# Kernel tuning notes

Hardware: AMD Instinct MI355X
Metric: run time of the kernel (lower is better)

The kernel has to match this reference:

```python
import jax, jax.numpy as jnp
import numpy as np

B, C, HW, NP, L, D, NH, OUT = 32, 3, 224, 14, 12, 768, 12, 1000
PS = HW // NP            # 16
IN_D = C * PS * PS       # 768
S = NP * NP + 1          # 197
DH = D // NH             # 64
MD = 4 * D               # 3072


def setup_inputs() -> dict:
    key = jax.random.key(0)
    ks = iter(jax.random.split(key, 32))
    g = lambda shape: jax.random.normal(next(ks), shape, dtype=jnp.float32) * 0.02
    return {
        "images": jax.random.normal(next(ks), (B, C, HW, HW), dtype=jnp.float32),
        "Wp": g((D, IN_D)), "bp": jnp.zeros((D,), jnp.float32),
        "cls": jax.random.normal(next(ks), (1, D), dtype=jnp.float32),
        "pos": jnp.zeros((S, D), jnp.float32),  # frozen zeros in original
        "ln1_g": jnp.ones((L, D), jnp.float32), "ln1_b": jnp.zeros((L, D), jnp.float32),
        "Wq": g((L, NH, DH, DH)), "bq": jnp.zeros((L, NH, DH), jnp.float32),
        "Wk": g((L, NH, DH, DH)), "bk": jnp.zeros((L, NH, DH), jnp.float32),
        "Wv": g((L, NH, DH, DH)), "bv": jnp.zeros((L, NH, DH), jnp.float32),
        "ln2_g": jnp.ones((L, D), jnp.float32), "ln2_b": jnp.zeros((L, D), jnp.float32),
        "W1": g((L, MD, D)), "b1": jnp.zeros((L, MD), jnp.float32),
        "W2": g((L, D, MD)), "b2": jnp.zeros((L, D), jnp.float32),
        "Wh": g((OUT, D)), "bh": jnp.zeros((OUT,), jnp.float32),
    }


def _layernorm(x, g, b, eps=1e-5):
    m = jnp.mean(x, axis=-1, keepdims=True)
    v = jnp.var(x, axis=-1, keepdims=True)
    return (x - m) * jax.lax.rsqrt(v + eps) * g + b


def reference(images, Wp, bp, cls, pos, ln1_g, ln1_b, Wq, bq, Wk, bk, Wv, bv,
              ln2_g, ln2_b, W1, b1, W2, b2, Wh, bh):
    n = images.shape[0]
    # patchify: flatten order is (c, ph, pw) per patch, matching torch .flatten()
    p = images.reshape(n, C, NP, PS, NP, PS).transpose(0, 2, 4, 1, 3, 5)
    p = p.reshape(n, NP * NP, IN_D)
    tokens = p @ Wp.T + bp                                    # [B, NP^2, D]
    tokens = jnp.concatenate([jnp.broadcast_to(cls, (n, 1, D)), tokens], axis=1)
    x = tokens + pos                                          # [B, S, D]

    scale = 1.0 / np.sqrt(DH)

    def block(x, prm):
        g1, b1n, wq, bqv, wk, bkv, wv, bvv, g2, b2n, w1, b1v, w2, b2v = prm
        h = _layernorm(x, g1, b1n)
        hh = h.reshape(n, S, NH, DH)                          # split heads
        q = jnp.einsum('bshd,hed->bshe', hh, wq) + bqv
        k = jnp.einsum('bshd,hed->bshe', hh, wk) + bkv
        v = jnp.einsum('bshd,hed->bshe', hh, wv) + bvv
        att = jax.nn.softmax(jnp.einsum('bqhe,bkhe->bhqk', q, k) * scale, axis=-1)
        o = jnp.einsum('bhqk,bkhe->bqhe', att, v).reshape(n, S, D)
        x = x + o
        h2 = _layernorm(x, g2, b2n)
        m = jax.nn.gelu(h2 @ w1.T + b1v, approximate=False) @ w2.T + b2v
        return x + m, None

    x, _ = jax.lax.scan(block, x,
                        (ln1_g, ln1_b, Wq, bq, Wk, bk, Wv, bv,
                         ln2_g, ln2_b, W1, b1, W2, b2))
    logits = x[:, 0] @ Wh.T + bh
    return jax.nn.softmax(logits, axis=-1)
```

## Files before the change

### kernel.cpp

```cpp
#include <hip/hip_runtime.h>
#include <math.h>
#include <stdint.h>

#define NBATCH 32
#define SEQ 197
#define DIM 768
#define NHEAD 12
#define DH 64
#define MDIM 3072
#define NLAYER 12
#define NPATCH 196
#define NOUT 1000
#define MROWS (NBATCH * SEQ)
#define SPLITK 2

typedef __bf16 bf16x8 __attribute__((ext_vector_type(8)));
typedef float f32x4 __attribute__((ext_vector_type(4)));

__device__ __forceinline__ unsigned short f2bf(float f) {
    unsigned u = __float_as_uint(f);
    unsigned r = u + 0x7fffu + ((u >> 16) & 1u);
    return (unsigned short)(r >> 16);
}

__device__ __forceinline__ f32x4 mfma16(bf16x8 a, bf16x8 b, f32x4 c) {
    return __builtin_amdgcn_mfma_f32_16x16x32_bf16(a, b, c, 0, 0, 0);
}

__device__ __forceinline__ void gload_lds16(const void* g, const void* lds) {
    __builtin_amdgcn_global_load_lds(
        (const __attribute__((address_space(1))) void*)(uintptr_t)g,
        (__attribute__((address_space(3))) void*)(uint32_t)(uintptr_t)lds,
        16, 0, 0);
}

#define WAIT_VMCNT_4() asm volatile("s_waitcnt vmcnt(4)" ::: "memory")
#define WAIT_VMCNT_0() asm volatile("s_waitcnt vmcnt(0)" ::: "memory")
#define BARRIER_RAW()                      \
    do {                                   \
        asm volatile("" ::: "memory");     \
        __builtin_amdgcn_s_barrier();      \
        asm volatile("" ::: "memory");     \
    } while (0)

__global__ __launch_bounds__(256) void cvt4(const float* __restrict__ src,
                                            unsigned short* __restrict__ dst, int n4) {
    int stride = gridDim.x * 256;
    for (int i = blockIdx.x * 256 + threadIdx.x; i < n4; i += stride) {
        float4 f = *(const float4*)(src + (size_t)i * 4);
        ushort4 o;
        o.x = f2bf(f.x); o.y = f2bf(f.y); o.z = f2bf(f.z); o.w = f2bf(f.w);
        *(ushort4*)(dst + (size_t)i * 4) = o;
    }
}

__global__ __launch_bounds__(256) void cvt_qkvw(const float* __restrict__ Wq,
                                                const float* __restrict__ Wk,
                                                const float* __restrict__ Wv,
                                                unsigned short* __restrict__ dst) {
    const int n = NLAYER * NHEAD * 3 * 64 * 64;
    int stride = gridDim.x * 256;
    for (int i = blockIdx.x * 256 + threadIdx.x; i < n; i += stride) {
        int d = i & 63, e = (i >> 6) & 63;
        int v = i >> 12;
        int t = v % 3, hh = (v / 3) % NHEAD, l = v / (3 * NHEAD);
        const float* src = (t == 0) ? Wq : (t == 1) ? Wk : Wv;
        dst[i] = f2bf(src[(((size_t)(l * NHEAD + hh)) * 64 + e) * 64 + d]);
    }
}

__global__ __launch_bounds__(256) void cls_pos_kernel(const float* __restrict__ cls,
                                                      const float* __restrict__ pos,
                                                      float* __restrict__ x) {
    int b = blockIdx.x, tid = threadIdx.x;
#pragma unroll
    for (int i = 0; i < 3; i++) {
        int c = tid + i * 256;
        x[(size_t)b * SEQ * DIM + c] = cls[c] + pos[c];
    }
}

__global__ __launch_bounds__(256) void gemm_patch_bf(const unsigned short* __restrict__ imgbf,
                                                     const unsigned short* __restrict__ wpbf,
                                                     const float* __restrict__ bp,
                                                     const float* __restrict__ pos,
                                                     float* __restrict__ x) {
    __shared__ __align__(16) unsigned short As[2][128 * 32];
    __shared__ __align__(16) unsigned short Bs[2][128 * 32];
    const int t = threadIdx.x, l = t & 63, w = t >> 6;
    const int bm = blockIdx.x * 128, bn = blockIdx.y * 128;
    const int wr = w >> 1, wc = w & 1;
    f32x4 acc[4][4] = {};

    const int ra0 = t >> 2, ka0 = (t & 3) * 8;
    const int ra1 = (t + 256) >> 2, ka1 = ((t + 256) & 3) * 8;
    int gm0 = bm + ra0, b0 = gm0 / NPATCH, p0 = gm0 % NPATCH;
    int gm1 = bm + ra1, b1 = gm1 / NPATCH, p1 = gm1 % NPATCH;
    const unsigned short* ib0 =
        imgbf + ((size_t)b0 * 3 * 224 + (size_t)(p0 / 14) * 16) * 224 + (p0 % 14) * 16;
    const unsigned short* ib1 =
        imgbf + ((size_t)b1 * 3 * 224 + (size_t)(p1 / 14) * 16) * 224 + (p1 % 14) * 16;
    const unsigned short* Br0 = wpbf + (size_t)(bn + ra0) * 768 + ka0;
    const unsigned short* Br1 = wpbf + (size_t)(bn + ra1) * 768 + ka1;
    const int lA0 = (0 * 256 + w * 64) * 8, lA1 = (1 * 256 + w * 64) * 8;
    const int lr = l & 15, lk = (l >> 4) * 8;

#define PATCH_STAGE(buf, k0)                                                   \
    {                                                                          \
        int kA0 = (k0) + ka0, kA1 = (k0) + ka1;                                \
        int c0 = kA0 >> 8, i0 = (kA0 >> 4) & 15, j0 = kA0 & 15;                \
        int c1 = kA1 >> 8, i1 = (kA1 >> 4) & 15, j1 = kA1 & 15;                \
        gload_lds16(ib0 + ((size_t)c0 * 224 + i0) * 224 + j0, As[buf] + lA0);  \
        gload_lds16(ib1 + ((size_t)c1 * 224 + i1) * 224 + j1, As[buf] + lA1);  \
        gload_lds16(Br0 + (k0), Bs[buf] + lA0);                                \
        gload_lds16(Br1 + (k0), Bs[buf] + lA1);                                \
    }

    PATCH_STAGE(0, 0);
    int cur = 0;
    for (int k0 = 0; k0 < 768; k0 += 32) {
        if (k0 + 32 < 768) {
            PATCH_STAGE(cur ^ 1, k0 + 32);
            WAIT_VMCNT_4();
        } else {
            WAIT_VMCNT_0();
        }
        BARRIER_RAW();
        bf16x8 a[4], bfr[4];
#pragma unroll
        for (int m = 0; m < 4; m++)
            a[m] = *(const bf16x8*)(As[cur] + (wr * 64 + m * 16 + lr) * 32 + lk);
#pragma unroll
        for (int n = 0; n < 4; n++)
            bfr[n] = *(const bf16x8*)(Bs[cur] + (wc * 64 + n * 16 + lr) * 32 + lk);
#pragma unroll
        for (int m = 0; m < 4; m++)
#pragma unroll
            for (int n = 0; n < 4; n++)
                acc[m][n] = mfma16(a[m], bfr[n], acc[m][n]);
        BARRIER_RAW();
        cur ^= 1;
    }
#undef PATCH_STAGE

#pragma unroll
    for (int m = 0; m < 4; m++) {
#pragma unroll
        for (int r = 0; r < 4; r++) {
            int gm = bm + wr * 64 + m * 16 + (l >> 4) * 4 + r;
            int b2 = gm / NPATCH, p2 = gm % NPATCH;
            size_t orow = (size_t)(b2 * SEQ + 1 + p2) * DIM;
#pragma unroll
            for (int n = 0; n < 4; n++) {
                int gn = bn + wc * 64 + n * 16 + lr;
                x[orow + gn] = acc[m][n][r] + bp[gn] + pos[(size_t)(1 + p2) * DIM + gn];
            }
        }
    }
}

template <int RES, int RED>
__global__ __launch_bounds__(256) void ln_wave(const float* __restrict__ x_in,
                                               const float* __restrict__ addv,
                                               float* __restrict__ x_out,
                                               unsigned short* __restrict__ h_out,
                                               const float* __restrict__ g,
                                               const float* __restrict__ bb,
                                               const float* __restrict__ parts,
                                               const float* __restrict__ badd) {
    int w = threadIdx.x >> 6, l = threadIdx.x & 63;
    size_t row = (size_t)blockIdx.x * 4 + w;
    const float* xr = x_in + row * DIM;
    float4 v[3];
    float s = 0.f;
#pragma unroll
    for (int u = 0; u < 3; u++) {
        int c = u * 256 + l * 4;
        v[u] = *(const float4*)(xr + c);
        if (RES) {
            float4 a4 = *(const float4*)(addv + row * DIM + c);
            v[u].x += a4.x; v[u].y += a4.y; v[u].z += a4.z; v[u].w += a4.w;
        }
        if (RED) {
            float4 b4 = *(const float4*)(badd + c);
            v[u].x += b4.x; v[u].y += b4.y; v[u].z += b4.z; v[u].w += b4.w;
#pragma unroll
            for (int kc = 0; kc < SPLITK; kc++) {
                float4 p4 = *(const float4*)(parts + ((size_t)kc * MROWS + row) * DIM + c);
                v[u].x += p4.x; v[u].y += p4.y; v[u].z += p4.z; v[u].w += p4.w;
            }
        }
        s += v[u].x + v[u].y + v[u].z + v[u].w;
    }
#pragma unroll
    for (int o = 1; o < 64; o <<= 1) s += __shfl_xor(s, o, 64);
    float mean = s * (1.0f / 768.0f);
    float s2 = 0.f;
#pragma unroll
    for (int u = 0; u < 3; u++) {
        float dx = v[u].x - mean, dy = v[u].y - mean, dz = v[u].z - mean, dw = v[u].w - mean;
        s2 += dx * dx + dy * dy + dz * dz + dw * dw;
    }
#pragma unroll
    for (int o = 1; o < 64; o <<= 1) s2 += __shfl_xor(s2, o, 64);
    float inv = rsqrtf(s2 * (1.0f / 768.0f) + 1e-5f);
#pragma unroll
    for (int u = 0; u < 3; u++) {
        int c = u * 256 + l * 4;
        float4 g4 = *(const float4*)(g + c);
        float4 b4 = *(const float4*)(bb + c);
        ushort4 o;
        o.x = f2bf((v[u].x - mean) * inv * g4.x + b4.x);
        o.y = f2bf((v[u].y - mean) * inv * g4.y + b4.y);
        o.z = f2bf((v[u].z - mean) * inv * g4.z + b4.z);
        o.w = f2bf((v[u].w - mean) * inv * g4.w + b4.w);
        *(ushort4*)(h_out + row * DIM + c) = o;
        if (RES || RED) *(float4*)(x_out + row * DIM + c) = v[u];
    }
}

__global__ __launch_bounds__(256) void reduceK(float* __restrict__ x,
                                               const float* __restrict__ parts,
                                               const float* __restrict__ badd) {
    int w = threadIdx.x >> 6, l = threadIdx.x & 63;
    size_t row = (size_t)blockIdx.x * 4 + w;
#pragma unroll
    for (int u = 0; u < 3; u++) {
        int c = u * 256 + l * 4;
        float4 v = *(const float4*)(x + row * DIM + c);
        float4 b4 = *(const float4*)(badd + c);
        v.x += b4.x; v.y += b4.y; v.z += b4.z; v.w += b4.w;
#pragma unroll
        for (int kc = 0; kc < SPLITK; kc++) {
            float4 p4 = *(const float4*)(parts + ((size_t)kc * MROWS + row) * DIM + c);
            v.x += p4.x; v.y += p4.y; v.z += p4.z; v.w += p4.w;
        }
        *(float4*)(x + row * DIM + c) = v;
    }
}

#define KS_OFF 0
#define QS_OFF 14400
#define VT_OFF 28800
#define RG_OFF 43648
#define WS_OFF (RG_OFF + 14400)

__global__ __launch_bounds__(512) void fused_attn(const unsigned short* __restrict__ hbf,
                                                  const unsigned short* __restrict__ wqkv,
                                                  const float* __restrict__ bq,
                                                  const float* __restrict__ bk,
                                                  const float* __restrict__ bv,
                                                  float* __restrict__ o) {
    __shared__ __align__(16) unsigned short lds[73344];
    const int b = blockIdx.x, hd = blockIdx.y;
    const int t = threadIdx.x, l = t & 63, w = t >> 6;
    const size_t base = ((size_t)b * SEQ) * DIM + hd * DH;
    const int lr = l & 15, lk4 = l >> 4;
    const unsigned short* wh = wqkv + (size_t)hd * 12288;

    for (int i = t; i < 197 * 16; i += 512) {
        int s = i >> 4, c4 = i & 15;
        ushort4 v4 = *(const ushort4*)(hbf + base + (size_t)s * DIM + c4 * 4);
        *(ushort4*)(lds + RG_OFF + s * 72 + c4 * 4) = v4;
    }
    if (t < 48) {
        int s = 197 + (t >> 4), c4 = t & 15;
        ushort4 z; z.x = 0; z.y = 0; z.z = 0; z.w = 0;
        *(ushort4*)(lds + RG_OFF + s * 72 + c4 * 4) = z;
    }
    for (int i = t; i < 192 * 16; i += 512) {
        int r = i >> 4, c4 = i & 15;
        ushort4 v4 = *(const ushort4*)(wh + (size_t)r * 64 + c4 * 4);
        *(ushort4*)(lds + WS_OFF + r * 72 + c4 * 4) = v4;
    }
    for (int i = t; i < 64 * 32; i += 512) {
        int d = i >> 5, s2 = 197 + (i & 31);
        if (s2 < 232) lds[VT_OFF + d * 232 + s2] = 0;
    }
    __syncthreads();

    for (int st = w; st < 13; st += 8) {
        bf16x8 a0 = *(const bf16x8*)(lds + RG_OFF + (st * 16 + lr) * 72 + lk4 * 8);
        bf16x8 a1 = *(const bf16x8*)(lds + RG_OFF + (st * 16 + lr) * 72 + 32 + lk4 * 8);
#pragma unroll
        for (int tt = 0; tt < 3; tt++) {
            const float* bias = (tt == 0) ? bq : (tt == 1) ? bk : bv;
#pragma unroll
            for (int et = 0; et < 4; et++) {
                int wrow = (tt * 64 + et * 16 + lr) * 72;
                bf16x8 b0 = *(const bf16x8*)(lds + WS_OFF + wrow + lk4 * 8);
                bf16x8 b1 = *(const bf16x8*)(lds + WS_OFF + wrow + 32 + lk4 * 8);
                f32x4 acc = {0.f, 0.f, 0.f, 0.f};
                acc = mfma16(a0, b0, acc);
                acc = mfma16(a1, b1, acc);
                int e = et * 16 + lr;
                float bval = bias[hd * 64 + e];
#pragma unroll
                for (int r = 0; r < 4; r++) {
                    int s = st * 16 + lk4 * 4 + r;
                    if (s < SEQ) {
                        unsigned short val = f2bf(acc[r] + bval);
                        if (tt == 0) lds[QS_OFF + s * 72 + e] = val;
                        else if (tt == 1) lds[KS_OFF + s * 72 + e] = val;
                        else lds[VT_OFF + e * 232 + s] = val;
                    }
                }
            }
        }
    }
    __syncthreads();

    const int Pb = RG_OFF + w * 3712;
    {
        int jj = 208 + lk4 * 4;
        lds[Pb + lr * 232 + jj + 0] = 0;
        lds[Pb + lr * 232 + jj + 1] = 0;
        lds[Pb + lr * 232 + jj + 2] = 0;
        lds[Pb + lr * 232 + jj + 3] = 0;
    }

    for (int qt = w; qt < 13; qt += 8) {
        int qrow = min(qt * 16 + lr, SEQ - 1);
        bf16x8 q0 = *(const bf16x8*)(lds + QS_OFF + qrow * 72 + lk4 * 8);
        bf16x8 q1 = *(const bf16x8*)(lds + QS_OFF + qrow * 72 + 32 + lk4 * 8);
        f32x4 st_[13];
#pragma unroll
        for (int jt = 0; jt < 13; jt++) st_[jt] = (f32x4){0.f, 0.f, 0.f, 0.f};
#pragma unroll
        for (int jt = 0; jt < 13; jt++) {
            int jrow = min(jt * 16 + lr, SEQ - 1);
            bf16x8 k0 = *(const bf16x8*)(lds + KS_OFF + jrow * 72 + lk4 * 8);
            bf16x8 k1 = *(const bf16x8*)(lds + KS_OFF + jrow * 72 + 32 + lk4 * 8);
            st_[jt] = mfma16(k0, q0, st_[jt]);
            st_[jt] = mfma16(k1, q1, st_[jt]);
        }
        float mx = -1e30f;
#pragma unroll
        for (int jt = 0; jt < 13; jt++)
#pragma unroll
            for (int r = 0; r < 4; r++) {
                int j = jt * 16 + lk4 * 4 + r;
                float sv = st_[jt][r] * 0.125f;
                st_[jt][r] = (j < SEQ) ? sv : -1e30f;
                mx = fmaxf(mx, st_[jt][r]);
            }
        mx = fmaxf(mx, __shfl_xor(mx, 16, 64));
        mx = fmaxf(mx, __shfl_xor(mx, 32, 64));
        float sum = 0.f;
#pragma unroll
        for (int jt = 0; jt < 13; jt++)
#pragma unroll
            for (int r = 0; r < 4; r++) {
                float p = __expf(st_[jt][r] - mx);
                st_[jt][r] = p;
                sum += p;
            }
        sum += __shfl_xor(sum, 16, 64);
        sum += __shfl_xor(sum, 32, 64);
        float inv = 1.0f / sum;
#pragma unroll
        for (int jt = 0; jt < 13; jt++) {
            ushort4 pk;
            pk.x = f2bf(st_[jt][0] * inv); pk.y = f2bf(st_[jt][1] * inv);
            pk.z = f2bf(st_[jt][2] * inv); pk.w = f2bf(st_[jt][3] * inv);
            *(ushort4*)(lds + Pb + lr * 232 + jt * 16 + lk4 * 4) = pk;
        }
        f32x4 acc[4] = {};
#pragma unroll
        for (int kt = 0; kt < 7; kt++) {
            bf16x8 pa = *(const bf16x8*)(lds + Pb + lr * 232 + kt * 32 + lk4 * 8);
#pragma unroll
            for (int nt = 0; nt < 4; nt++) {
                bf16x8 bv8 = *(const bf16x8*)(lds + VT_OFF + (nt * 16 + lr) * 232 + kt * 32 + lk4 * 8);
                acc[nt] = mfma16(pa, bv8, acc[nt]);
            }
        }
#pragma unroll
        for (int nt = 0; nt < 4; nt++)
#pragma unroll
            for (int r = 0; r < 4; r++) {
                int qq = qt * 16 + lk4 * 4 + r;
                if (qq < SEQ) o[base + (size_t)qq * DIM + nt * 16 + lr] = acc[nt][r];
            }
    }
}

template <int MODE, int SWAPXY>
__global__ __launch_bounds__(256) void gemm_bf(const unsigned short* __restrict__ A,
                                               const unsigned short* __restrict__ Bw,
                                               const float* __restrict__ bias,
                                               void* __restrict__ Cout,
                                               const float* __restrict__ res,
                                               int M, int N, int K) {
    __shared__ __align__(16) unsigned short As[2][128 * 32];
    __shared__ __align__(16) unsigned short Bs[2][128 * 32];
    const int t = threadIdx.x, l = t & 63, w = t >> 6;
    const int bm = (SWAPXY ? blockIdx.y : blockIdx.x) * 128;
    const int bn = (SWAPXY ? blockIdx.x : blockIdx.y) * 128;
    const int wr = w >> 1, wc = w & 1;
    f32x4 acc[4][4] = {};

    const int ra0 = t >> 2, ka0 = (t & 3) * 8;
    const int ra1 = (t + 256) >> 2, ka1 = ((t + 256) & 3) * 8;
    const unsigned short* Ar0 = A + (size_t)min(bm + ra0, M - 1) * K + ka0;
    const unsigned short* Ar1 = A + (size_t)min(bm + ra1, M - 1) * K + ka1;
    const unsigned short* Br0 = Bw + (size_t)(bn + ra0) * K + ka0;
    const unsigned short* Br1 = Bw + (size_t)(bn + ra1) * K + ka1;
    const int lo0 = (0 * 256 + w * 64) * 8, lo1 = (1 * 256 + w * 64) * 8;
    const int lr = l & 15, lk = (l >> 4) * 8;

    gload_lds16(Ar0, As[0] + lo0);
    gload_lds16(Ar1, As[0] + lo1);
    gload_lds16(Br0, Bs[0] + lo0);
    gload_lds16(Br1, Bs[0] + lo1);
    int cur = 0;
    for (int k0 = 0; k0 < K; k0 += 32) {
        if (k0 + 32 < K) {
            gload_lds16(Ar0 + k0 + 32, As[cur ^ 1] + lo0);
            gload_lds16(Ar1 + k0 + 32, As[cur ^ 1] + lo1);
            gload_lds16(Br0 + k0 + 32, Bs[cur ^ 1] + lo0);
            gload_lds16(Br1 + k0 + 32, Bs[cur ^ 1] + lo1);
            WAIT_VMCNT_4();
        } else {
            WAIT_VMCNT_0();
        }
        BARRIER_RAW();
        bf16x8 a[4], bfr[4];
#pragma unroll
        for (int m = 0; m < 4; m++)
            a[m] = *(const bf16x8*)(As[cur] + (wr * 64 + m * 16 + lr) * 32 + lk);
#pragma unroll
        for (int n = 0; n < 4; n++)
            bfr[n] = *(const bf16x8*)(Bs[cur] + (wc * 64 + n * 16 + lr) * 32 + lk);
#pragma unroll
        for (int m = 0; m < 4; m++)
#pragma unroll
            for (int n = 0; n < 4; n++)
                acc[m][n] = mfma16(a[m], bfr[n], acc[m][n]);
        BARRIER_RAW();
        cur ^= 1;
    }

#pragma unroll
    for (int m = 0; m < 4; m++) {
#pragma unroll
        for (int r = 0; r < 4; r++) {
            int gm = bm + wr * 64 + m * 16 + (l >> 4) * 4 + r;
            if (gm >= M) continue;
#pragma unroll
            for (int n = 0; n < 4; n++) {
                int gn = bn + wc * 64 + n * 16 + lr;
                float vb = acc[m][n][r] + bias[gn];
                if (MODE == 1) {
                    float gl = 0.5f * vb * (1.0f + erff(vb * 0.70710678118f));
                    ((unsigned short*)Cout)[(size_t)gm * N + gn] = f2bf(gl);
                } else {
                    ((float*)Cout)[(size_t)gm * N + gn] = vb + res[(size_t)gm * N + gn];
                }
            }
        }
    }
}

__global__ __launch_bounds__(256) void gemm_splitk(const unsigned short* __restrict__ A,
                                                   const unsigned short* __restrict__ Bw,
                                                   float* __restrict__ parts,
                                                   int M, int N, int KFULL) {
    __shared__ __align__(16) unsigned short As[2][128 * 32];
    __shared__ __align__(16) unsigned short Bs[2][128 * 32];
    const int t = threadIdx.x, l = t & 63, w = t >> 6;
    const int bm = blockIdx.x * 128, bn = blockIdx.y * 128;
    const int KC = KFULL / SPLITK;
    const int kbeg = blockIdx.z * KC;
    const int wr = w >> 1, wc = w & 1;
    f32x4 acc[4][4] = {};

    const int ra0 = t >> 2, ka0 = (t & 3) * 8;
    const int ra1 = (t + 256) >> 2, ka1 = ((t + 256) & 3) * 8;
    const unsigned short* Ar0 = A + (size_t)min(bm + ra0, M - 1) * KFULL + kbeg + ka0;
    const unsigned short* Ar1 = A + (size_t)min(bm + ra1, M - 1) * KFULL + kbeg + ka1;
    const unsigned short* Br0 = Bw + (size_t)(bn + ra0) * KFULL + kbeg + ka0;
    const unsigned short* Br1 = Bw + (size_t)(bn + ra1) * KFULL + kbeg + ka1;
    const int lo0 = (0 * 256 + w * 64) * 8, lo1 = (1 * 256 + w * 64) * 8;
    const int lr = l & 15, lk = (l >> 4) * 8;

    gload_lds16(Ar0, As[0] + lo0);
    gload_lds16(Ar1, As[0] + lo1);
    gload_lds16(Br0, Bs[0] + lo0);
    gload_lds16(Br1, Bs[0] + lo1);
    int cur = 0;
    for (int k0 = 0; k0 < KC; k0 += 32) {
        if (k0 + 32 < KC) {
            gload_lds16(Ar0 + k0 + 32, As[cur ^ 1] + lo0);
            gload_lds16(Ar1 + k0 + 32, As[cur ^ 1] + lo1);
            gload_lds16(Br0 + k0 + 32, Bs[cur ^ 1] + lo0);
            gload_lds16(Br1 + k0 + 32, Bs[cur ^ 1] + lo1);
            WAIT_VMCNT_4();
        } else {
            WAIT_VMCNT_0();
        }
        BARRIER_RAW();
        bf16x8 a[4], bfr[4];
#pragma unroll
        for (int m = 0; m < 4; m++)
            a[m] = *(const bf16x8*)(As[cur] + (wr * 64 + m * 16 + lr) * 32 + lk);
#pragma unroll
        for (int n = 0; n < 4; n++)
            bfr[n] = *(const bf16x8*)(Bs[cur] + (wc * 64 + n * 16 + lr) * 32 + lk);
#pragma unroll
        for (int m = 0; m < 4; m++)
#pragma unroll
            for (int n = 0; n < 4; n++)
                acc[m][n] = mfma16(a[m], bfr[n], acc[m][n]);
        BARRIER_RAW();
        cur ^= 1;
    }

    float* po = parts + (size_t)blockIdx.z * M * N;
#pragma unroll
    for (int m = 0; m < 4; m++) {
#pragma unroll
        for (int r = 0; r < 4; r++) {
            int gm = bm + wr * 64 + m * 16 + (l >> 4) * 4 + r;
            if (gm >= M) continue;
#pragma unroll
            for (int n = 0; n < 4; n++) {
                int gn = bn + wc * 64 + n * 16 + lr;
                po[(size_t)gm * N + gn] = acc[m][n][r];
            }
        }
    }
}

__global__ __launch_bounds__(256) void head_kernel(const float* __restrict__ x,
                                                   const float* __restrict__ Wh,
                                                   const float* __restrict__ bh,
                                                   float* __restrict__ logits) {
    __shared__ float xs[768];
    int b = blockIdx.x;
    int tid = threadIdx.x;
#pragma unroll
    for (int i = 0; i < 3; i++) xs[tid + i * 256] = x[(size_t)b * SEQ * DIM + tid + i * 256];
    __syncthreads();
    int wave = tid >> 6, lane = tid & 63;
    int o = blockIdx.y * 4 + wave;
    if (o < NOUT) {
        float acc = 0;
#pragma unroll
        for (int t = 0; t < 12; t++) {
            int d = lane + t * 64;
            acc = fmaf(xs[d], Wh[(size_t)o * DIM + d], acc);
        }
#pragma unroll
        for (int off = 32; off > 0; off >>= 1) acc += __shfl_down(acc, off, 64);
        if (lane == 0) logits[b * NOUT + o] = acc + bh[o];
    }
}

__global__ __launch_bounds__(256) void softmax_kernel(const float* __restrict__ logits,
                                                      float* __restrict__ out) {
    __shared__ float tmp[4];
    int b = blockIdx.x, tid = threadIdx.x;
    float vals[4];
    float mx = -1e30f;
#pragma unroll
    for (int i = 0; i < 4; i++) {
        int c = tid + i * 256;
        vals[i] = (c < NOUT) ? logits[b * NOUT + c] : -1e30f;
        mx = fmaxf(mx, vals[i]);
    }
#pragma unroll
    for (int o = 32; o > 0; o >>= 1) mx = fmaxf(mx, __shfl_down(mx, o, 64));
    int wave = tid >> 6, lane = tid & 63;
    __syncthreads();
    if (lane == 0) tmp[wave] = mx;
    __syncthreads();
    mx = fmaxf(fmaxf(tmp[0], tmp[1]), fmaxf(tmp[2], tmp[3]));
    float s = 0;
#pragma unroll
    for (int i = 0; i < 4; i++) {
        int c = tid + i * 256;
        if (c < NOUT) {
            vals[i] = __expf(vals[i] - mx);
            s += vals[i];
        } else vals[i] = 0.f;
    }
#pragma unroll
    for (int o = 32; o > 0; o >>= 1) s += __shfl_down(s, o, 64);
    __syncthreads();
    if (lane == 0) tmp[wave] = s;
    __syncthreads();
    s = tmp[0] + tmp[1] + tmp[2] + tmp[3];
    float invs = 1.0f / s;
#pragma unroll
    for (int i = 0; i < 4; i++) {
        int c = tid + i * 256;
        if (c < NOUT) out[b * NOUT + c] = vals[i] * invs;
    }
}

extern "C" void kernel_launch(void* const* d_in, const int* in_sizes, int n_in,
                              void* d_out, int out_size, void* d_ws, size_t ws_size,
                              hipStream_t stream) {
    const float* images = (const float*)d_in[0];
    const float* Wp   = (const float*)d_in[1];
    const float* bp   = (const float*)d_in[2];
    const float* cls  = (const float*)d_in[3];
    const float* pos  = (const float*)d_in[4];
    const float* ln1g = (const float*)d_in[5];
    const float* ln1b = (const float*)d_in[6];
    const float* Wq   = (const float*)d_in[7];
    const float* bq   = (const float*)d_in[8];
    const float* Wk   = (const float*)d_in[9];
    const float* bk   = (const float*)d_in[10];
    const float* Wv   = (const float*)d_in[11];
    const float* bv   = (const float*)d_in[12];
    const float* ln2g = (const float*)d_in[13];
    const float* ln2b = (const float*)d_in[14];
    const float* W1   = (const float*)d_in[15];
    const float* b1   = (const float*)d_in[16];
    const float* W2   = (const float*)d_in[17];
    const float* b2   = (const float*)d_in[18];
    const float* Wh   = (const float*)d_in[19];
    const float* bh   = (const float*)d_in[20];
    float* out = (float*)d_out;

    const size_t NX = (size_t)MROWS * DIM;
    const size_t NIMG = (size_t)NBATCH * 3 * 224 * 224;
    const size_t NW = (size_t)MDIM * DIM;

    char* p = (char*)d_ws;
    float* x      = (float*)p;            p += NX * 4;
    float* h      = (float*)p;            p += NX * 4;
    float* logits = (float*)p;            p += (size_t)NBATCH * NOUT * 4;
    unsigned short* hbf   = (unsigned short*)p; p += NX * 2;
    unsigned short* h2bf  = (unsigned short*)p; p += NX * 2;
    unsigned short* mid   = (unsigned short*)p; p += (size_t)MROWS * MDIM * 2;
    unsigned short* wqkvb = (unsigned short*)p; p += (size_t)NLAYER * NHEAD * 12288 * 2;
    unsigned short* imgbf = (unsigned short*)p; p += NIMG * 2;
    unsigned short* wpbf  = (unsigned short*)p; p += (size_t)DIM * DIM * 2;

    size_t used = (size_t)(p - (char*)d_ws);
    bool skq = ws_size >= used + (size_t)SPLITK * NX * 4;
    float* parts = (float*)p;
    if (skq) p += (size_t)SPLITK * NX * 4;
    used = (size_t)(p - (char*)d_ws);
    bool big = ws_size >= used + (size_t)2 * NLAYER * NW * 2;
    unsigned short* w1a = (unsigned short*)p;
    unsigned short* w2a = big ? w1a + (size_t)NLAYER * NW : w1a + NW;

    cls_pos_kernel<<<dim3(NBATCH), dim3(256), 0, stream>>>(cls, pos, x);
    cvt4<<<dim3(2048), dim3(256), 0, stream>>>(images, imgbf, (int)(NIMG / 4));
    cvt4<<<dim3(576), dim3(256), 0, stream>>>(Wp, wpbf, (int)(DIM * DIM / 4));
    cvt_qkvw<<<dim3(1024), dim3(256), 0, stream>>>(Wq, Wk, Wv, wqkvb);
    gemm_patch_bf<<<dim3(49, 6), dim3(256), 0, stream>>>(imgbf, wpbf, bp, pos, x);
    if (big) {
        cvt4<<<dim3(2048), dim3(256), 0, stream>>>(W1, w1a, (int)(NLAYER * NW / 4));
        cvt4<<<dim3(2048), dim3(256), 0, stream>>>(W2, w2a, (int)(NLAYER * NW / 4));
    }

    for (int l = 0; l < NLAYER; l++) {
        const unsigned short* wl1 = big ? w1a + (size_t)l * NW : w1a;
        const unsigned short* wl2 = big ? w2a + (size_t)l * NW : w2a;
        if (!big) {
            cvt4<<<dim3(2048), dim3(256), 0, stream>>>(W1 + (size_t)l * NW, w1a, (int)(NW / 4));
            cvt4<<<dim3(2048), dim3(256), 0, stream>>>(W2 + (size_t)l * NW, w1a + NW, (int)(NW / 4));
        }
        if (skq && l > 0) {
            ln_wave<0, 1><<<dim3(MROWS / 4), dim3(256), 0, stream>>>(
                x, nullptr, x, hbf, ln1g + l * DIM, ln1b + l * DIM, parts, b2 + (l - 1) * DIM);
        } else {
            ln_wave<0, 0><<<dim3(MROWS / 4), dim3(256), 0, stream>>>(
                x, nullptr, nullptr, hbf, ln1g + l * DIM, ln1b + l * DIM, nullptr, nullptr);
        }
        fused_attn<<<dim3(NBATCH, NHEAD), dim3(512), 0, stream>>>(
            hbf, wqkvb + (size_t)l * NHEAD * 12288,
            bq + l * NHEAD * DH, bk + l * NHEAD * DH, bv + l * NHEAD * DH, h);
        ln_wave<1, 0><<<dim3(MROWS / 4), dim3(256), 0, stream>>>(
            x, h, x, h2bf, ln2g + l * DIM, ln2b + l * DIM, nullptr, nullptr);
        gemm_bf<1, 1><<<dim3(24, 50), dim3(256), 0, stream>>>(
            h2bf, wl1, b1 + l * MDIM, mid, nullptr, MROWS, MDIM, DIM);
        if (skq) {
            gemm_splitk<<<dim3(50, 6, SPLITK), dim3(256), 0, stream>>>(
                mid, wl2, parts, MROWS, DIM, MDIM);
        } else {
            gemm_bf<2, 0><<<dim3(50, 6), dim3(256), 0, stream>>>(
                mid, wl2, b2 + l * DIM, x, x, MROWS, DIM, MDIM);
        }
    }
    if (skq) {
        reduceK<<<dim3(MROWS / 4), dim3(256), 0, stream>>>(x, parts, b2 + (NLAYER - 1) * DIM);
    }

    head_kernel<<<dim3(NBATCH, 250), dim3(256), 0, stream>>>(x, Wh, bh, logits);
    softmax_kernel<<<dim3(NBATCH), dim3(256), 0, stream>>>(logits, out);
}
```

Baseline: 2.257 ms.

## Compute only CLS token in final layer after attention

In the last layer only the CLS row feeds the classifier head. So the attention kernel computes queries and the output for the first query tile only. The second LayerNorm and both MLP GEMMs then run on just the 32 CLS rows, which are gathered with a row stride of SEQ. The final split-K reduction is folded into the head kernel, which removes the reduceK pass over all rows. This is legitimate dead-work elimination, but it depends on the split-K path being active and on the MLP GEMMs handling M=32 correctly.

```diff
diff --git a/kernel.cpp b/kernel.cpp
--- a/kernel.cpp
+++ b/kernel.cpp
@@ -167,10 +167,12 @@
                                                const float* __restrict__ g,
                                                const float* __restrict__ bb,
                                                const float* __restrict__ parts,
-                                               const float* __restrict__ badd) {
+                                               const float* __restrict__ badd,
+                                               int xmul) {
     int w = threadIdx.x >> 6, l = threadIdx.x & 63;
     size_t row = (size_t)blockIdx.x * 4 + w;
-    const float* xr = x_in + row * DIM;
+    size_t xrow = row * xmul;
+    const float* xr = x_in + xrow * DIM;
     float4 v[3];
     float s = 0.f;
 #pragma unroll
@@ -178,7 +180,7 @@
         int c = u * 256 + l * 4;
         v[u] = *(const float4*)(xr + c);
         if (RES) {
-            float4 a4 = *(const float4*)(addv + row * DIM + c);
+            float4 a4 = *(const float4*)(addv + xrow * DIM + c);
             v[u].x += a4.x; v[u].y += a4.y; v[u].z += a4.z; v[u].w += a4.w;
         }
         if (RED) {
@@ -215,27 +217,7 @@
         o.z = f2bf((v[u].z - mean) * inv * g4.z + b4.z);
         o.w = f2bf((v[u].w - mean) * inv * g4.w + b4.w);
         *(ushort4*)(h_out + row * DIM + c) = o;
-        if (RES || RED) *(float4*)(x_out + row * DIM + c) = v[u];
-    }
-}
-
-__global__ __launch_bounds__(256) void reduceK(float* __restrict__ x,
-                                               const float* __restrict__ parts,
-                                               const float* __restrict__ badd) {
-    int w = threadIdx.x >> 6, l = threadIdx.x & 63;
-    size_t row = (size_t)blockIdx.x * 4 + w;
-#pragma unroll
-    for (int u = 0; u < 3; u++) {
-        int c = u * 256 + l * 4;
-        float4 v = *(const float4*)(x + row * DIM + c);
-        float4 b4 = *(const float4*)(badd + c);
-        v.x += b4.x; v.y += b4.y; v.z += b4.z; v.w += b4.w;
-#pragma unroll
-        for (int kc = 0; kc < SPLITK; kc++) {
-            float4 p4 = *(const float4*)(parts + ((size_t)kc * MROWS + row) * DIM + c);
-            v.x += p4.x; v.y += p4.y; v.z += p4.z; v.w += p4.w;
-        }
-        *(float4*)(x + row * DIM + c) = v;
+        if (RES || RED) *(float4*)(x_out + xrow * DIM + c) = v[u];
     }
 }
 
@@ -245,6 +227,7 @@
 #define RG_OFF 43648
 #define WS_OFF (RG_OFF + 14400)
 
+template <int QTMAX>
 __global__ __launch_bounds__(512) void fused_attn(const unsigned short* __restrict__ hbf,
                                                   const unsigned short* __restrict__ wqkv,
                                                   const float* __restrict__ bq,
@@ -284,6 +267,7 @@
         bf16x8 a1 = *(const bf16x8*)(lds + RG_OFF + (st * 16 + lr) * 72 + 32 + lk4 * 8);
 #pragma unroll
         for (int tt = 0; tt < 3; tt++) {
+            if (QTMAX == 1 && tt == 0 && st >= QTMAX) continue;
             const float* bias = (tt == 0) ? bq : (tt == 1) ? bk : bv;
 #pragma unroll
             for (int et = 0; et < 4; et++) {
@@ -319,7 +303,7 @@
         lds[Pb + lr * 232 + jj + 3] = 0;
     }
 
-    for (int qt = w; qt < 13; qt += 8) {
+    for (int qt = w; qt < QTMAX; qt += 8) {
         int qrow = min(qt * 16 + lr, SEQ - 1);
         bf16x8 q0 = *(const bf16x8*)(lds + QS_OFF + qrow * 72 + lk4 * 8);
         bf16x8 q1 = *(const bf16x8*)(lds + QS_OFF + qrow * 72 + 32 + lk4 * 8);
@@ -535,12 +519,23 @@
 __global__ __launch_bounds__(256) void head_kernel(const float* __restrict__ x,
                                                    const float* __restrict__ Wh,
                                                    const float* __restrict__ bh,
-                                                   float* __restrict__ logits) {
+                                                   float* __restrict__ logits,
+                                                   const float* __restrict__ cparts,
+                                                   const float* __restrict__ b2l) {
     __shared__ float xs[768];
     int b = blockIdx.x;
     int tid = threadIdx.x;
 #pragma unroll
-    for (int i = 0; i < 3; i++) xs[tid + i * 256] = x[(size_t)b * SEQ * DIM + tid + i * 256];
+    for (int i = 0; i < 3; i++) {
+        int c = tid + i * 256;
+        float v = x[(size_t)b * SEQ * DIM + c];
+        if (cparts) {
+            v += b2l[c];
+            v += cparts[(size_t)b * DIM + c];
+            v += cparts[(size_t)NBATCH * DIM + (size_t)b * DIM + c];
+        }
+        xs[c] = v;
+    }
     __syncthreads();
     int wave = tid >> 6, lane = tid & 63;
     int o = blockIdx.y * 4 + wave;
@@ -668,30 +663,42 @@
         }
         if (skq && l > 0) {
             ln_wave<0, 1><<<dim3(MROWS / 4), dim3(256), 0, stream>>>(
-                x, nullptr, x, hbf, ln1g + l * DIM, ln1b + l * DIM, parts, b2 + (l - 1) * DIM);
+                x, nullptr, x, hbf, ln1g + l * DIM, ln1b + l * DIM, parts, b2 + (l - 1) * DIM, 1);
         } else {
             ln_wave<0, 0><<<dim3(MROWS / 4), dim3(256), 0, stream>>>(
-                x, nullptr, nullptr, hbf, ln1g + l * DIM, ln1b + l * DIM, nullptr, nullptr);
-        }
-        fused_attn<<<dim3(NBATCH, NHEAD), dim3(512), 0, stream>>>(
-            hbf, wqkvb + (size_t)l * NHEAD * 12288,
-            bq + l * NHEAD * DH, bk + l * NHEAD * DH, bv + l * NHEAD * DH, h);
-        ln_wave<1, 0><<<dim3(MROWS / 4), dim3(256), 0, stream>>>(
-            x, h, x, h2bf, ln2g + l * DIM, ln2b + l * DIM, nullptr, nullptr);
-        gemm_bf<1, 1><<<dim3(24, 50), dim3(256), 0, stream>>>(
-            h2bf, wl1, b1 + l * MDIM, mid, nullptr, MROWS, MDIM, DIM);
-        if (skq) {
-            gemm_splitk<<<dim3(50, 6, SPLITK), dim3(256), 0, stream>>>(
-                mid, wl2, parts, MROWS, DIM, MDIM);
+                x, nullptr, nullptr, hbf, ln1g + l * DIM, ln1b + l * DIM, nullptr, nullptr, 1);
+        }
+        bool last = skq && (l == NLAYER - 1);
+        if (last) {
+            fused_attn<1><<<dim3(NBATCH, NHEAD), dim3(512), 0, stream>>>(
+                hbf, wqkvb + (size_t)l * NHEAD * 12288,
+                bq + l * NHEAD * DH, bk + l * NHEAD * DH, bv + l * NHEAD * DH, h);
+            ln_wave<1, 0><<<dim3(NBATCH / 4), dim3(256), 0, stream>>>(
+                x, h, x, h2bf, ln2g + l * DIM, ln2b + l * DIM, nullptr, nullptr, SEQ);
+            gemm_bf<1, 1><<<dim3(24, 1), dim3(256), 0, stream>>>(
+                h2bf, wl1, b1 + l * MDIM, mid, nullptr, NBATCH, MDIM, DIM);
+            gemm_splitk<<<dim3(1, 6, SPLITK), dim3(256), 0, stream>>>(
+                mid, wl2, parts, NBATCH, DIM, MDIM);
         } else {
-            gemm_bf<2, 0><<<dim3(50, 6), dim3(256), 0, stream>>>(
-                mid, wl2, b2 + l * DIM, x, x, MROWS, DIM, MDIM);
-        }
-    }
-    if (skq) {
-        reduceK<<<dim3(MROWS / 4), dim3(256), 0, stream>>>(x, parts, b2 + (NLAYER - 1) * DIM);
-    }
-
-    head_kernel<<<dim3(NBATCH, 250), dim3(256), 0, stream>>>(x, Wh, bh, logits);
+            fused_attn<13><<<dim3(NBATCH, NHEAD), dim3(512), 0, stream>>>(
+                hbf, wqkvb + (size_t)l * NHEAD * 12288,
+                bq + l * NHEAD * DH, bk + l * NHEAD * DH, bv + l * NHEAD * DH, h);
+            ln_wave<1, 0><<<dim3(MROWS / 4), dim3(256), 0, stream>>>(
+                x, h, x, h2bf, ln2g + l * DIM, ln2b + l * DIM, nullptr, nullptr, 1);
+            gemm_bf<1, 1><<<dim3(24, 50), dim3(256), 0, stream>>>(
+                h2bf, wl1, b1 + l * MDIM, mid, nullptr, MROWS, MDIM, DIM);
+            if (skq) {
+                gemm_splitk<<<dim3(50, 6, SPLITK), dim3(256), 0, stream>>>(
+                    mid, wl2, parts, MROWS, DIM, MDIM);
+            } else {
+                gemm_bf<2, 0><<<dim3(50, 6), dim3(256), 0, stream>>>(
+                    mid, wl2, b2 + l * DIM, x, x, MROWS, DIM, MDIM);
+            }
+        }
+    }
+
+    head_kernel<<<dim3(NBATCH, 250), dim3(256), 0, stream>>>(
+        x, Wh, bh, logits,
+        skq ? parts : nullptr, skq ? b2 + (NLAYER - 1) * DIM : nullptr);
     softmax_kernel<<<dim3(NBATCH), dim3(256), 0, stream>>>(logits, out);
 }
```

Result: faster. 2.152 ms (-4.7%).
